# Kernel tuning notes

Measured on AMD Instinct MI355X. Metric: run time of the kernel, lower is better.

The kernel has to match this reference:

```python
import jax, jax.numpy as jnp
import numpy as np

STIM_KER_LEN = 50  # length of causal stimulus kernel
K_BASIS = 2        # number of exponential basis functions in history kernel


def setup_inputs() -> dict:
    key = jax.random.key(0)
    T, NTR = 8192, 1024
    k0, k1, k2 = jax.random.split(key, 3)
    t = jnp.arange(T, dtype=jnp.float32)                    # uniform grid, dt = 1.0
    stim = jax.random.normal(k0, (T,), jnp.float32)
    rand = jax.random.uniform(k1, (T, NTR), jnp.float32)    # per-step uniforms (torch.rand in loop)
    # learned parameters
    bias = jnp.array([-4.0], jnp.float32)                   # nn.Parameter bias
    k_stim = jax.random.normal(k2, (STIM_KER_LEN,), jnp.float32) * 0.1  # stim kernel weights
    hist_w = jnp.array([-5.0, 1.0], jnp.float32)            # exponential basis coefficients
    hist_tau = jnp.array([5.0, 20.0], jnp.float32)          # exponential basis time constants
    return dict(t=t, stim=stim, rand=rand, bias=bias, k_stim=k_stim,
                hist_w=hist_w, hist_tau=hist_tau)


def reference(t, stim, rand, bias, k_stim, hist_w, hist_tau):
    dt = t[1] - t[0]
    T = t.shape[0]
    ntr = rand.shape[1]
    # stim_kernel(stim, dt): causal convolution scaled by dt, then shift_tensor(..., 1, fill=0)
    stim_conv = jnp.convolve(stim, k_stim)[:T] * dt                       # (T,)
    stim_conv = jnp.concatenate([jnp.zeros((1,), stim.dtype), stim_conv[:-1]])
    # history kernel: ker(s) = sum_k hist_w[k] * exp(-s / hist_tau[k]), evaluated from 0
    # one step after each spike -> linear recurrence on per-basis state s (K, ntr).
    decay = jnp.exp(-dt / hist_tau)                                        # (K,)

    def step(s, inp):
        sc_j, r_j = inp                       # scalar, (ntr,)
        hist_j = jnp.sum(s, axis=0)           # (ntr,) == hist_conv[j]
        loglam_j = bias[0] + sc_j + hist_j    # (ntr,)
        p_spk = 1.0 - jnp.exp(-jnp.exp(loglam_j) * dt)
        spk_j = p_spk > r_j                   # (ntr,) bool
        s_new = decay[:, None] * s + hist_w[:, None] * spk_j.astype(s.dtype)
        return s_new, (loglam_j, spk_j)

    s0 = jnp.zeros((hist_w.shape[0], ntr), jnp.float32)
    _, (log_lam, mask_spikes) = jax.lax.scan(step, s0, (stim_conv, rand))
    return log_lam, mask_spikes
```

## Files before the change

### kernel.cpp

```cpp
#include <hip/hip_runtime.h>
#include <math.h>

#define T_LEN 8192
#define NTRIALS 1024
#define TN ((size_t)T_LEN * NTRIALS)
#define KLEN 50
#define CHUNK 256
#define NCHUNK (T_LEN / CHUNK)
#define FARW 256
#define NEARW 256
#define WARM (FARW + NEARW)
#define PF 32
#define BAND 1e-4f

__global__ void prep_basc_kernel(const float* __restrict__ t,
                                 const float* __restrict__ stim,
                                 const float* __restrict__ bias,
                                 const float* __restrict__ k_stim,
                                 const float* __restrict__ hist_w,
                                 const float* __restrict__ hist_tau,
                                 double* __restrict__ dparams,
                                 double* __restrict__ basc,
                                 float* __restrict__ bascf) {
  int j = blockIdx.x * blockDim.x + threadIdx.x;
  if (j >= T_LEN) return;
  double dt = (double)t[1] - (double)t[0];
  if (j == 0) {
    dparams[0] = exp(-dt / (double)hist_tau[0]);
    dparams[1] = exp(-dt / (double)hist_tau[1]);
    dparams[2] = (double)hist_w[0];
    dparams[3] = (double)hist_w[1];
    dparams[4] = dt;
    basc[0] = (double)bias[0];
    bascf[0] = (float)(double)bias[0];
    return;
  }
  int n = j - 1;
  int mmax = n < (KLEN - 1) ? n : (KLEN - 1);
  double acc = 0.0;
  for (int m = 0; m <= mmax; ++m)
    acc += (double)k_stim[m] * (double)stim[n - m];
  double v = (double)bias[0] + dt * acc;
  basc[j] = v;
  bascf[j] = (float)v;
}

__global__ void prep_thr32_kernel(const float* __restrict__ rnd,
                                  const float* __restrict__ bascf,
                                  const double* __restrict__ dparams,
                                  float* __restrict__ thr32) {
  size_t m = ((size_t)blockIdx.x * blockDim.x + threadIdx.x) * 4;
  float dtf = (float)dparams[4];
  float4 r4 = *reinterpret_cast<const float4*>(rnd + m);
  float b = bascf[m >> 10];
  float4 o;
  o.x = logf(-log1pf(-r4.x) / dtf) - b;
  o.y = logf(-log1pf(-r4.y) / dtf) - b;
  o.z = logf(-log1pf(-r4.z) / dtf) - b;
  o.w = logf(-log1pf(-r4.w) / dtf) - b;
  *reinterpret_cast<float4*>(thr32 + m) = o;
}

__device__ __noinline__ bool decide64(const float* __restrict__ rnd,
                                      const double* __restrict__ basc,
                                      double dt, int j, int i, double h) {
  double r = (double)rnd[(size_t)j * NTRIALS + i];
  double t = log(-log1p(-r) / dt) - basc[j];
  return h > t;
}

__global__ __launch_bounds__(64, 1) void spec_scan2_kernel(
    const float* __restrict__ thr, const float* __restrict__ rnd,
    const double* __restrict__ basc, const float* __restrict__ bascf,
    const double* __restrict__ dparams, float* __restrict__ out) {
  const int tid = threadIdx.x;
  const int tb  = blockIdx.x & 15;
  const int c   = blockIdx.x >> 4;
  const int i   = tb * 64 + tid;
  const double d0 = dparams[0], d1 = dparams[1];
  const double w0 = dparams[2], w1 = dparams[3];
  const double dt = dparams[4];
  const float d0f = (float)d0, d1f = (float)d1;
  const float w0f = (float)w0, w1f = (float)w1;

  const int jstart = c * CHUNK;
  const int nw    = jstart < WARM ? jstart : WARM;
  const int jw    = jstart - nw;
  const int nearn = nw < NEARW ? nw : NEARW;
  const int farn  = nw - nearn;
  const int j1    = jw + farn;

  const float* __restrict__ p = thr + i;
  float bufA[PF], bufB[PF];
#pragma unroll
  for (int k = 0; k < PF; ++k) bufA[k] = p[(size_t)(jw + k) * NTRIALS];
  __builtin_amdgcn_sched_barrier(0);

  float a0 = 0.0f, a1 = 0.0f;
  for (int q = 0; q < farn; q += 2 * PF) {
    const int j0 = jw + q;
#pragma unroll
    for (int k = 0; k < PF; ++k) bufB[k] = p[(size_t)(j0 + PF + k) * NTRIALS];
    __builtin_amdgcn_sched_barrier(0);
#pragma unroll
    for (int k = 0; k < PF; ++k) {
      float h = a0 + a1;
      bool s = h > bufA[k];
      a0 = fmaf(d0f, a0, s ? w0f : 0.0f);
      a1 = fmaf(d1f, a1, s ? w1f : 0.0f);
    }
    __builtin_amdgcn_sched_barrier(0);
#pragma unroll
    for (int k = 0; k < PF; ++k) bufA[k] = p[(size_t)(j0 + 2 * PF + k) * NTRIALS];
    __builtin_amdgcn_sched_barrier(0);
#pragma unroll
    for (int k = 0; k < PF; ++k) {
      float h = a0 + a1;
      bool s = h > bufB[k];
      a0 = fmaf(d0f, a0, s ? w0f : 0.0f);
      a1 = fmaf(d1f, a1, s ? w1f : 0.0f);
    }
    __builtin_amdgcn_sched_barrier(0);
  }

  double s0 = (double)a0, s1 = (double)a1;
  for (int q = 0; q < nearn; q += 2 * PF) {
    const int j0 = j1 + q;
#pragma unroll
    for (int k = 0; k < PF; ++k) bufB[k] = p[(size_t)(j0 + PF + k) * NTRIALS];
    __builtin_amdgcn_sched_barrier(0);
#pragma unroll
    for (int k = 0; k < PF; ++k) {
      double h = s0 + s1;
      float d = (float)h - bufA[k];
      bool s = d > 0.0f;
      if (__builtin_expect(fabsf(d) < BAND, 0))
        s = decide64(rnd, basc, dt, j0 + k, i, h);
      s0 = fma(d0, s0, s ? w0 : 0.0);
      s1 = fma(d1, s1, s ? w1 : 0.0);
    }
    __builtin_amdgcn_sched_barrier(0);
#pragma unroll
    for (int k = 0; k < PF; ++k) bufA[k] = p[(size_t)(j0 + 2 * PF + k) * NTRIALS];
    __builtin_amdgcn_sched_barrier(0);
#pragma unroll
    for (int k = 0; k < PF; ++k) {
      double h = s0 + s1;
      float d = (float)h - bufB[k];
      bool s = d > 0.0f;
      if (__builtin_expect(fabsf(d) < BAND, 0))
        s = decide64(rnd, basc, dt, j0 + PF + k, i, h);
      s0 = fma(d0, s0, s ? w0 : 0.0);
      s1 = fma(d1, s1, s ? w1 : 0.0);
    }
    __builtin_amdgcn_sched_barrier(0);
  }

  float* __restrict__ po_ll = out + (size_t)jstart * NTRIALS + i;
  float* __restrict__ po_mk = po_ll + TN;
  for (int q = 0; q < CHUNK; q += 2 * PF) {
    const int j0 = jstart + q;
#pragma unroll
    for (int k = 0; k < PF; ++k) bufB[k] = p[(size_t)(j0 + PF + k) * NTRIALS];
    __builtin_amdgcn_sched_barrier(0);
#pragma unroll
    for (int k = 0; k < PF; ++k) {
      double h = s0 + s1;
      float d = (float)h - bufA[k];
      bool s = d > 0.0f;
      if (__builtin_expect(fabsf(d) < BAND, 0))
        s = decide64(rnd, basc, dt, j0 + k, i, h);
      po_ll[(size_t)(q + k) * NTRIALS] = (float)h + bascf[j0 + k];
      po_mk[(size_t)(q + k) * NTRIALS] = s ? 1.0f : 0.0f;
      s0 = fma(d0, s0, s ? w0 : 0.0);
      s1 = fma(d1, s1, s ? w1 : 0.0);
    }
    __builtin_amdgcn_sched_barrier(0);
    if (q + 2 * PF < CHUNK) {
#pragma unroll
      for (int k = 0; k < PF; ++k)
        bufA[k] = p[(size_t)(j0 + 2 * PF + k) * NTRIALS];
    }
    __builtin_amdgcn_sched_barrier(0);
#pragma unroll
    for (int k = 0; k < PF; ++k) {
      double h = s0 + s1;
      float d = (float)h - bufB[k];
      bool s = d > 0.0f;
      if (__builtin_expect(fabsf(d) < BAND, 0))
        s = decide64(rnd, basc, dt, j0 + PF + k, i, h);
      po_ll[(size_t)(q + PF + k) * NTRIALS] = (float)h + bascf[j0 + PF + k];
      po_mk[(size_t)(q + PF + k) * NTRIALS] = s ? 1.0f : 0.0f;
      s0 = fma(d0, s0, s ? w0 : 0.0);
      s1 = fma(d1, s1, s ? w1 : 0.0);
    }
    __builtin_amdgcn_sched_barrier(0);
  }
}

__global__ __launch_bounds__(64, 1) void glm_scan_inline_kernel(
    const float* __restrict__ rnd, const double* __restrict__ basc,
    const double* __restrict__ dparams, float* __restrict__ out) {
  const int i = blockIdx.x * 64 + threadIdx.x;
  const double d0 = dparams[0], d1 = dparams[1];
  const double w0 = dparams[2], w1 = dparams[3];
  const double dt = dparams[4];
  double s0 = 0.0, s1 = 0.0;
  float* __restrict__ out_ll = out;
  float* __restrict__ out_mk = out + TN;
  for (int j = 0; j < T_LEN; ++j) {
    double r = (double)rnd[(size_t)j * NTRIALS + i];
    double th = log(-log1p(-r) / dt) - basc[j];
    double hist = s0 + s1;
    bool spk = hist > th;
    out_ll[(size_t)j * NTRIALS + i] = (float)(basc[j] + hist);
    out_mk[(size_t)j * NTRIALS + i] = spk ? 1.0f : 0.0f;
    s0 = fma(d0, s0, spk ? w0 : 0.0);
    s1 = fma(d1, s1, spk ? w1 : 0.0);
  }
}

extern "C" void kernel_launch(void* const* d_in, const int* in_sizes, int n_in,
                              void* d_out, int out_size, void* d_ws, size_t ws_size,
                              hipStream_t stream) {
  const float* t        = (const float*)d_in[0];
  const float* stim     = (const float*)d_in[1];
  const float* rnd      = (const float*)d_in[2];
  const float* bias     = (const float*)d_in[3];
  const float* k_stim   = (const float*)d_in[4];
  const float* hist_w   = (const float*)d_in[5];
  const float* hist_tau = (const float*)d_in[6];
  float* out = (float*)d_out;

  char* ws = (char*)d_ws;
  const size_t off_bascf = 64;
  const size_t off_basc  = off_bascf + (size_t)T_LEN * 4;
  const size_t off_thr   = off_basc + (size_t)T_LEN * 8;
  const size_t need_full = off_thr + TN * 4;
  const size_t need_min  = off_thr;

  double* dparams = (double*)ws;
  float*  bascf   = (float*)(ws + off_bascf);
  double* basc    = (double*)(ws + off_basc);
  float*  thr32   = (float*)(ws + off_thr);

  prep_basc_kernel<<<(T_LEN + 255) / 256, 256, 0, stream>>>(
      t, stim, bias, k_stim, hist_w, hist_tau, dparams, basc, bascf);

  if (ws_size >= need_full) {
    prep_thr32_kernel<<<(int)(TN / 4 / 256), 256, 0, stream>>>(
        rnd, bascf, dparams, thr32);
    spec_scan2_kernel<<<NCHUNK * 16, 64, 0, stream>>>(
        thr32, rnd, basc, bascf, dparams, out);
  } else if (ws_size >= need_min) {
    glm_scan_inline_kernel<<<NTRIALS / 64, 64, 0, stream>>>(rnd, basc, dparams, out);
  }
}
```

Measured before the change: 92.45 us.

## Shrink scan chunks to 64 steps and fuse prep kernels into one launch

Cuts the speculative scan chunk from 256 to 64 time steps, so each block re-warms over the same 512-step window but emits fewer outputs. This gives 4x more blocks (2048) for parallelism on the GPU, at the cost of much more redundant warm-up work. It also merges the stimulus-convolution prep and the threshold prep into one kernel, one block per time step, which removes a launch and the dependency between the two prep kernels. The fallback path now computes the convolution inline and no longer needs workspace.

```diff
diff --git a/kernel.cpp b/kernel.cpp
--- a/kernel.cpp
+++ b/kernel.cpp
@@ -5,7 +5,7 @@
 #define NTRIALS 1024
 #define TN ((size_t)T_LEN * NTRIALS)
 #define KLEN 50
-#define CHUNK 256
+#define CHUNK 64
 #define NCHUNK (T_LEN / CHUNK)
 #define FARW 256
 #define NEARW 256
@@ -13,51 +13,47 @@
 #define PF 32
 #define BAND 1e-4f
 
-__global__ void prep_basc_kernel(const float* __restrict__ t,
-                                 const float* __restrict__ stim,
-                                 const float* __restrict__ bias,
-                                 const float* __restrict__ k_stim,
-                                 const float* __restrict__ hist_w,
-                                 const float* __restrict__ hist_tau,
-                                 double* __restrict__ dparams,
-                                 double* __restrict__ basc,
-                                 float* __restrict__ bascf) {
-  int j = blockIdx.x * blockDim.x + threadIdx.x;
-  if (j >= T_LEN) return;
-  double dt = (double)t[1] - (double)t[0];
-  if (j == 0) {
-    dparams[0] = exp(-dt / (double)hist_tau[0]);
-    dparams[1] = exp(-dt / (double)hist_tau[1]);
-    dparams[2] = (double)hist_w[0];
-    dparams[3] = (double)hist_w[1];
-    dparams[4] = dt;
-    basc[0] = (double)bias[0];
-    bascf[0] = (float)(double)bias[0];
-    return;
-  }
-  int n = j - 1;
-  int mmax = n < (KLEN - 1) ? n : (KLEN - 1);
+__global__ __launch_bounds__(256) void prep_fused_kernel(
+    const float* __restrict__ t, const float* __restrict__ stim,
+    const float* __restrict__ bias, const float* __restrict__ k_stim,
+    const float* __restrict__ hist_w, const float* __restrict__ hist_tau,
+    const float* __restrict__ rnd, double* __restrict__ dparams,
+    double* __restrict__ basc, float* __restrict__ bascf,
+    float* __restrict__ thr32) {
+  const int j = blockIdx.x;
+  const int tid = threadIdx.x;
+  const double dt = (double)t[1] - (double)t[0];
+
   double acc = 0.0;
-  for (int m = 0; m <= mmax; ++m)
-    acc += (double)k_stim[m] * (double)stim[n - m];
-  double v = (double)bias[0] + dt * acc;
-  basc[j] = v;
-  bascf[j] = (float)v;
-}
-
-__global__ void prep_thr32_kernel(const float* __restrict__ rnd,
-                                  const float* __restrict__ bascf,
-                                  const double* __restrict__ dparams,
-                                  float* __restrict__ thr32) {
-  size_t m = ((size_t)blockIdx.x * blockDim.x + threadIdx.x) * 4;
-  float dtf = (float)dparams[4];
+  if (j > 0) {
+    int n = j - 1;
+    int mmax = n < (KLEN - 1) ? n : (KLEN - 1);
+    for (int m = 0; m <= mmax; ++m)
+      acc += (double)k_stim[m] * (double)stim[n - m];
+  }
+  double b64 = (double)bias[0] + (j > 0 ? dt * acc : 0.0);
+  float bf = (float)b64;
+
+  if (tid == 0) {
+    basc[j] = b64;
+    bascf[j] = bf;
+    if (j == 0) {
+      dparams[0] = exp(-dt / (double)hist_tau[0]);
+      dparams[1] = exp(-dt / (double)hist_tau[1]);
+      dparams[2] = (double)hist_w[0];
+      dparams[3] = (double)hist_w[1];
+      dparams[4] = dt;
+    }
+  }
+
+  const float dtf = (float)dt;
+  size_t m = (size_t)j * NTRIALS + (size_t)tid * 4;
   float4 r4 = *reinterpret_cast<const float4*>(rnd + m);
-  float b = bascf[m >> 10];
   float4 o;
-  o.x = logf(-log1pf(-r4.x) / dtf) - b;
-  o.y = logf(-log1pf(-r4.y) / dtf) - b;
-  o.z = logf(-log1pf(-r4.z) / dtf) - b;
-  o.w = logf(-log1pf(-r4.w) / dtf) - b;
+  o.x = logf(-log1pf(-r4.x) / dtf) - bf;
+  o.y = logf(-log1pf(-r4.y) / dtf) - bf;
+  o.z = logf(-log1pf(-r4.z) / dtf) - bf;
+  o.w = logf(-log1pf(-r4.w) / dtf) - bf;
   *reinterpret_cast<float4*>(thr32 + m) = o;
 }
 
@@ -69,7 +65,7 @@
   return h > t;
 }
 
-__global__ __launch_bounds__(64, 1) void spec_scan2_kernel(
+__global__ __launch_bounds__(64, 1) void spec_scan3_kernel(
     const float* __restrict__ thr, const float* __restrict__ rnd,
     const double* __restrict__ basc, const float* __restrict__ bascf,
     const double* __restrict__ dparams, float* __restrict__ out) {
@@ -158,62 +154,63 @@
 
   float* __restrict__ po_ll = out + (size_t)jstart * NTRIALS + i;
   float* __restrict__ po_mk = po_ll + TN;
-  for (int q = 0; q < CHUNK; q += 2 * PF) {
-    const int j0 = jstart + q;
-#pragma unroll
-    for (int k = 0; k < PF; ++k) bufB[k] = p[(size_t)(j0 + PF + k) * NTRIALS];
-    __builtin_amdgcn_sched_barrier(0);
-#pragma unroll
-    for (int k = 0; k < PF; ++k) {
-      double h = s0 + s1;
-      float d = (float)h - bufA[k];
-      bool s = d > 0.0f;
-      if (__builtin_expect(fabsf(d) < BAND, 0))
-        s = decide64(rnd, basc, dt, j0 + k, i, h);
-      po_ll[(size_t)(q + k) * NTRIALS] = (float)h + bascf[j0 + k];
-      po_mk[(size_t)(q + k) * NTRIALS] = s ? 1.0f : 0.0f;
-      s0 = fma(d0, s0, s ? w0 : 0.0);
-      s1 = fma(d1, s1, s ? w1 : 0.0);
-    }
-    __builtin_amdgcn_sched_barrier(0);
-    if (q + 2 * PF < CHUNK) {
-#pragma unroll
-      for (int k = 0; k < PF; ++k)
-        bufA[k] = p[(size_t)(j0 + 2 * PF + k) * NTRIALS];
-    }
-    __builtin_amdgcn_sched_barrier(0);
-#pragma unroll
-    for (int k = 0; k < PF; ++k) {
-      double h = s0 + s1;
-      float d = (float)h - bufB[k];
-      bool s = d > 0.0f;
-      if (__builtin_expect(fabsf(d) < BAND, 0))
-        s = decide64(rnd, basc, dt, j0 + PF + k, i, h);
-      po_ll[(size_t)(q + PF + k) * NTRIALS] = (float)h + bascf[j0 + PF + k];
-      po_mk[(size_t)(q + PF + k) * NTRIALS] = s ? 1.0f : 0.0f;
-      s0 = fma(d0, s0, s ? w0 : 0.0);
-      s1 = fma(d1, s1, s ? w1 : 0.0);
-    }
-    __builtin_amdgcn_sched_barrier(0);
+#pragma unroll
+  for (int k = 0; k < PF; ++k) bufB[k] = p[(size_t)(jstart + PF + k) * NTRIALS];
+  __builtin_amdgcn_sched_barrier(0);
+#pragma unroll
+  for (int k = 0; k < PF; ++k) {
+    double h = s0 + s1;
+    float d = (float)h - bufA[k];
+    bool s = d > 0.0f;
+    if (__builtin_expect(fabsf(d) < BAND, 0))
+      s = decide64(rnd, basc, dt, jstart + k, i, h);
+    po_ll[(size_t)k * NTRIALS] = (float)h + bascf[jstart + k];
+    po_mk[(size_t)k * NTRIALS] = s ? 1.0f : 0.0f;
+    s0 = fma(d0, s0, s ? w0 : 0.0);
+    s1 = fma(d1, s1, s ? w1 : 0.0);
+  }
+  __builtin_amdgcn_sched_barrier(0);
+#pragma unroll
+  for (int k = 0; k < PF; ++k) {
+    double h = s0 + s1;
+    float d = (float)h - bufB[k];
+    bool s = d > 0.0f;
+    if (__builtin_expect(fabsf(d) < BAND, 0))
+      s = decide64(rnd, basc, dt, jstart + PF + k, i, h);
+    po_ll[(size_t)(PF + k) * NTRIALS] = (float)h + bascf[jstart + PF + k];
+    po_mk[(size_t)(PF + k) * NTRIALS] = s ? 1.0f : 0.0f;
+    s0 = fma(d0, s0, s ? w0 : 0.0);
+    s1 = fma(d1, s1, s ? w1 : 0.0);
   }
 }
 
 __global__ __launch_bounds__(64, 1) void glm_scan_inline_kernel(
-    const float* __restrict__ rnd, const double* __restrict__ basc,
-    const double* __restrict__ dparams, float* __restrict__ out) {
+    const float* __restrict__ rnd, const float* __restrict__ t,
+    const float* __restrict__ stim, const float* __restrict__ bias,
+    const float* __restrict__ k_stim, const float* __restrict__ hist_w,
+    const float* __restrict__ hist_tau, float* __restrict__ out) {
   const int i = blockIdx.x * 64 + threadIdx.x;
-  const double d0 = dparams[0], d1 = dparams[1];
-  const double w0 = dparams[2], w1 = dparams[3];
-  const double dt = dparams[4];
+  const double dt = (double)t[1] - (double)t[0];
+  const double d0 = exp(-dt / (double)hist_tau[0]);
+  const double d1 = exp(-dt / (double)hist_tau[1]);
+  const double w0 = (double)hist_w[0], w1 = (double)hist_w[1];
   double s0 = 0.0, s1 = 0.0;
   float* __restrict__ out_ll = out;
   float* __restrict__ out_mk = out + TN;
   for (int j = 0; j < T_LEN; ++j) {
+    double acc = 0.0;
+    if (j > 0) {
+      int n = j - 1;
+      int mmax = n < (KLEN - 1) ? n : (KLEN - 1);
+      for (int m = 0; m <= mmax; ++m)
+        acc += (double)k_stim[m] * (double)stim[n - m];
+    }
+    double b = (double)bias[0] + dt * acc;
     double r = (double)rnd[(size_t)j * NTRIALS + i];
-    double th = log(-log1p(-r) / dt) - basc[j];
+    double th = log(-log1p(-r) / dt) - b;
     double hist = s0 + s1;
     bool spk = hist > th;
-    out_ll[(size_t)j * NTRIALS + i] = (float)(basc[j] + hist);
+    out_ll[(size_t)j * NTRIALS + i] = (float)(b + hist);
     out_mk[(size_t)j * NTRIALS + i] = spk ? 1.0f : 0.0f;
     s0 = fma(d0, s0, spk ? w0 : 0.0);
     s1 = fma(d1, s1, spk ? w1 : 0.0);
@@ -237,22 +234,19 @@
   const size_t off_basc  = off_bascf + (size_t)T_LEN * 4;
   const size_t off_thr   = off_basc + (size_t)T_LEN * 8;
   const size_t need_full = off_thr + TN * 4;
-  const size_t need_min  = off_thr;
 
   double* dparams = (double*)ws;
   float*  bascf   = (float*)(ws + off_bascf);
   double* basc    = (double*)(ws + off_basc);
   float*  thr32   = (float*)(ws + off_thr);
 
-  prep_basc_kernel<<<(T_LEN + 255) / 256, 256, 0, stream>>>(
-      t, stim, bias, k_stim, hist_w, hist_tau, dparams, basc, bascf);
-
   if (ws_size >= need_full) {
-    prep_thr32_kernel<<<(int)(TN / 4 / 256), 256, 0, stream>>>(
-        rnd, bascf, dparams, thr32);
-    spec_scan2_kernel<<<NCHUNK * 16, 64, 0, stream>>>(
+    prep_fused_kernel<<<T_LEN, 256, 0, stream>>>(
+        t, stim, bias, k_stim, hist_w, hist_tau, rnd, dparams, basc, bascf, thr32);
+    spec_scan3_kernel<<<NCHUNK * 16, 64, 0, stream>>>(
         thr32, rnd, basc, bascf, dparams, out);
-  } else if (ws_size >= need_min) {
-    glm_scan_inline_kernel<<<NTRIALS / 64, 64, 0, stream>>>(rnd, basc, dparams, out);
-  }
-}
+  } else {
+    glm_scan_inline_kernel<<<NTRIALS / 64, 64, 0, stream>>>(
+        rnd, t, stim, bias, k_stim, hist_w, hist_tau, out);
+  }
+}
```

After: 101.2 us. 1.09x slower.
